# Performance work log

Measured on AMD Instinct MI355X. Metric: run time of the kernel, lower is better.

Reference implementation:

```python
import jax, jax.numpy as jnp
import numpy as np


def setup_inputs() -> dict:
    key = jax.random.key(0)
    k1, k2 = jax.random.split(key)
    num_tokens, top_k, num_experts = 1048576, 8, 64
    top_scores = jax.random.uniform(k1, (num_tokens, top_k), dtype=jnp.float32)
    selected_experts_indices = jax.random.randint(
        k2, (num_tokens, top_k), 0, num_experts, dtype=jnp.int64
    ) if jax.config.jax_enable_x64 else jax.random.randint(
        k2, (num_tokens, top_k), 0, num_experts, dtype=jnp.int32
    )
    return {
        "top_scores": top_scores,
        "selected_experts_indices": selected_experts_indices,
        "num_experts": num_experts,
    }


def reference(top_scores, selected_experts_indices, num_experts):
    flat_idx = selected_experts_indices.reshape(-1)  # [num_tokens*top_k]
    # histogram of tokens per expert (torch.histc returns float)
    num_tokens_per_expert = jnp.bincount(flat_idx, length=num_experts).astype(jnp.float32)
    # stable argsort by expert id -> permutation grouping tokens by expert
    token_indices_experts_sorted = jnp.argsort(flat_idx, stable=True)
    # gather routing scores into expert-sorted order
    top_scores_experts_sorted = top_scores.reshape(-1)[token_indices_experts_sorted]
    return (
        top_scores_experts_sorted,
        token_indices_experts_sorted,
        num_tokens_per_expert,
    )
```

## Files before the change

kernel.cpp:

```cpp
#include <hip/hip_runtime.h>


#define TILE 2048
#define WCH  512
#define RND  8

__device__ __forceinline__ unsigned long long match_mask(
    unsigned key,
    unsigned long long b0, unsigned long long b1, unsigned long long b2,
    unsigned long long b3, unsigned long long b4, unsigned long long b5,
    unsigned long long am) {
  unsigned long long m = am;
  m &= (key & 1u)  ? b0 : ~b0;
  m &= (key & 2u)  ? b1 : ~b1;
  m &= (key & 4u)  ? b2 : ~b2;
  m &= (key & 8u)  ? b3 : ~b3;
  m &= (key & 16u) ? b4 : ~b4;
  m &= (key & 32u) ? b5 : ~b5;
  return m;
}

__global__ __launch_bounds__(256) void hist_kernel(
    const int* __restrict__ idx, unsigned* __restrict__ countsT,
    int N, int nb) {
  __shared__ unsigned h[4][64];
  int wave = threadIdx.x >> 6;
  int lane = threadIdx.x & 63;
  h[wave][lane] = 0;
  __syncthreads();

  long long base = (long long)blockIdx.x * TILE;
  long long rem = (long long)N - base;
  if (rem >= TILE) {
    const int4* v = (const int4*)(idx + base);
    #pragma unroll
    for (int k = 0; k < TILE / 1024; ++k) {
      int4 x = v[threadIdx.x + k * 256];
      atomicAdd(&h[wave][((unsigned)x.x) & 63u], 1u);
      atomicAdd(&h[wave][((unsigned)x.y) & 63u], 1u);
      atomicAdd(&h[wave][((unsigned)x.z) & 63u], 1u);
      atomicAdd(&h[wave][((unsigned)x.w) & 63u], 1u);
    }
  } else if (rem > 0) {
    for (int j = threadIdx.x; j < (int)rem; j += 256)
      atomicAdd(&h[wave][((unsigned)idx[base + j]) & 63u], 1u);
  }
  __syncthreads();
  if (threadIdx.x < 64) {
    countsT[(size_t)threadIdx.x * nb + blockIdx.x] =
        h[0][threadIdx.x] + h[1][threadIdx.x] + h[2][threadIdx.x] + h[3][threadIdx.x];
  }
}

__global__ __launch_bounds__(256) void scan_kernel(
    unsigned* __restrict__ countsT, unsigned* __restrict__ totals,
    float* __restrict__ out_counts, int nb) {
  int e = blockIdx.x;
  int t = threadIdx.x;
  unsigned* row = countsT + (size_t)e * nb;
  int per = (nb + 255) >> 8;
  int base = t * per;

  unsigned s = 0;
  for (int j = 0; j < per; ++j) {
    int w = base + j;
    if (w < nb) s += row[w];
  }
  __shared__ unsigned sh[256];
  sh[t] = s;
  __syncthreads();
  for (int d = 1; d < 256; d <<= 1) {
    unsigned v = sh[t];
    unsigned a = (t >= d) ? sh[t - d] : 0u;
    __syncthreads();
    sh[t] = v + a;
    __syncthreads();
  }
  unsigned incl = sh[t];
  unsigned run = incl - s;
  for (int j = 0; j < per; ++j) {
    int w = base + j;
    if (w < nb) { unsigned v = row[w]; row[w] = run; run += v; }
  }
  if (t == 255) {
    totals[e] = incl;
    out_counts[e] = (float)incl;
  }
}

__global__ __launch_bounds__(256) void scatter_kernel(
    const int* __restrict__ idx, const float* __restrict__ scores,
    const unsigned* __restrict__ baseT, const unsigned* __restrict__ totals,
    float* __restrict__ out_scores, float* __restrict__ out_idx,
    int N, int nb) {
  __shared__ unsigned shc[4][64];
  __shared__ unsigned dbase[64];
  __shared__ float    ssc[TILE];
  __shared__ unsigned spk[TILE];

  const int wave = threadIdx.x >> 6;
  const int lane = threadIdx.x & 63;
  const unsigned long long lt = (1ull << lane) - 1ull;

  long long start = (long long)blockIdx.x * TILE + (long long)wave * WCH;
  long long remain = (long long)N - start;
  int full = 0;
  if (remain >= WCH) full = RND;
  else if (remain > 0) full = (int)(remain >> 6);
  bool hastail = (full < RND) && (remain > (long long)full * 64);

  unsigned rank_pk[2] = {0, 0};
  unsigned cnt_pk[2]  = {0, 0};
  unsigned e_pk[2]    = {0, 0};
  unsigned wtotal = 0;

  #pragma unroll
  for (int r = 0; r < RND; ++r) {
    if (r >= full) break;
    long long i = start + (long long)r * 64 + lane;
    unsigned e = ((unsigned)idx[i]) & 63u;
    unsigned long long b0 = __ballot(e & 1u);
    unsigned long long b1 = __ballot(e & 2u);
    unsigned long long b2 = __ballot(e & 4u);
    unsigned long long b3 = __ballot(e & 8u);
    unsigned long long b4 = __ballot(e & 16u);
    unsigned long long b5 = __ballot(e & 32u);
    unsigned long long ms = match_mask(e, b0, b1, b2, b3, b4, b5, ~0ull);
    unsigned long long ml = match_mask((unsigned)lane, b0, b1, b2, b3, b4, b5, ~0ull);
    unsigned rank = (unsigned)__popcll(ms & lt);
    unsigned cnt  = (unsigned)__popcll(ml);
    int q = r >> 2, sh = (r & 3) * 8;
    rank_pk[q] |= rank << sh;
    cnt_pk[q]  |= cnt << sh;
    e_pk[q]    |= e << sh;
    wtotal += cnt;
  }
  if (hastail) {
    int r = full;
    long long i = start + (long long)r * 64 + lane;
    bool valid = i < (long long)N;
    unsigned long long am = __ballot(valid ? 1 : 0);
    unsigned e = valid ? (((unsigned)idx[i]) & 63u) : 0u;
    unsigned long long b0 = __ballot(e & 1u);
    unsigned long long b1 = __ballot(e & 2u);
    unsigned long long b2 = __ballot(e & 4u);
    unsigned long long b3 = __ballot(e & 8u);
    unsigned long long b4 = __ballot(e & 16u);
    unsigned long long b5 = __ballot(e & 32u);
    unsigned long long ms = match_mask(e, b0, b1, b2, b3, b4, b5, am);
    unsigned long long ml = match_mask((unsigned)lane, b0, b1, b2, b3, b4, b5, am);
    unsigned rank = (unsigned)__popcll(ms & lt);
    unsigned cnt  = (unsigned)__popcll(ml);
    int q = r >> 2, sh = (r & 3) * 8;
    rank_pk[q] |= rank << sh;
    cnt_pk[q]  |= cnt << sh;
    e_pk[q]    |= e << sh;
    wtotal += cnt;
  }
  shc[wave][lane] = wtotal;
  __syncthreads();

  unsigned c0 = shc[0][lane], c1 = shc[1][lane], c2 = shc[2][lane], c3 = shc[3][lane];
  unsigned bc = c0 + c1 + c2 + c3;
  unsigned sum = bc;
  #pragma unroll
  for (int d = 1; d < 64; d <<= 1) {
    unsigned nv = __shfl_up(sum, d, 64);
    if (lane >= d) sum += nv;
  }
  unsigned local_start = sum - bc;
  unsigned running = local_start + (wave > 0 ? c0 : 0u) + (wave > 1 ? c1 : 0u) +
                     (wave > 2 ? c2 : 0u);

  if (threadIdx.x < 64) {
    unsigned tot = totals[lane];
    unsigned s2 = tot;
    #pragma unroll
    for (int d = 1; d < 64; d <<= 1) {
      unsigned nv = __shfl_up(s2, d, 64);
      if (lane >= d) s2 += nv;
    }
    unsigned estart = s2 - tot;
    unsigned gb0 = baseT[(size_t)lane * nb + blockIdx.x];
    dbase[lane] = estart + gb0 - local_start;
  }

  #pragma unroll
  for (int r = 0; r < RND; ++r) {
    if (r >= full) break;
    long long i = start + (long long)r * 64 + lane;
    float s = scores[i];
    int q = r >> 2, sh = (r & 3) * 8;
    unsigned e    = (e_pk[q] >> sh) & 0xffu;
    unsigned rank = (rank_pk[q] >> sh) & 0xffu;
    unsigned cnt  = (cnt_pk[q] >> sh) & 0xffu;
    unsigned old = (unsigned)__shfl((int)running, (int)e, 64);
    unsigned pos = old + rank;
    running += cnt;
    ssc[pos] = s;
    spk[pos] = (((unsigned)i) << 6) | e;
  }
  if (hastail) {
    int r = full;
    long long i = start + (long long)r * 64 + lane;
    bool valid = i < (long long)N;
    float s = valid ? scores[i] : 0.0f;
    int q = r >> 2, sh = (r & 3) * 8;
    unsigned e    = (e_pk[q] >> sh) & 0xffu;
    unsigned rank = (rank_pk[q] >> sh) & 0xffu;
    unsigned cnt  = (cnt_pk[q] >> sh) & 0xffu;
    unsigned old = (unsigned)__shfl((int)running, (int)e, 64);
    unsigned pos = old + rank;
    running += cnt;
    if (valid) {
      ssc[pos] = s;
      spk[pos] = (((unsigned)i) << 6) | e;
    }
  }
  __syncthreads();

  {
    long long bstart = (long long)blockIdx.x * TILE;
    long long rem = (long long)N - bstart;
    int bvalid = rem < TILE ? (int)rem : TILE;
    for (int j = threadIdx.x; j < bvalid; j += 256) {
      unsigned p = spk[j];
      unsigned e = p & 63u;
      unsigned d = dbase[e] + (unsigned)j;
      out_scores[d] = ssc[j];
      out_idx[d] = (float)(p >> 6);
    }
  }
}

extern "C" void kernel_launch(void* const* d_in, const int* in_sizes, int n_in,
                              void* d_out, int out_size, void* d_ws, size_t ws_size,
                              hipStream_t stream) {
  const float* scores = (const float*)d_in[0];
  const int* idx = (const int*)d_in[1];
  int N = in_sizes[0];

  float* out_scores = (float*)d_out;
  float* out_idx = out_scores + N;
  float* out_counts = out_idx + N;

  int nb = (N + TILE - 1) / TILE;
  unsigned* countsT = (unsigned*)d_ws;
  unsigned* totals = countsT + (size_t)64 * nb;

  hist_kernel<<<nb, 256, 0, stream>>>(idx, countsT, N, nb);
  scan_kernel<<<64, 256, 0, stream>>>(countsT, totals, out_counts, nb);
  scatter_kernel<<<nb, 256, 0, stream>>>(idx, scores, countsT, totals,
                                         out_scores, out_idx, N, nb);
}
```

Before: 158.7 us.

## Scatter into per-wave local segments to drop mid-kernel block barrier

The scatter kernel now has each wave lay out its own 512-element segment of shared memory sorted by expert, using only an intra-wave prefix scan. The block-wide histogram combine moves after the local scatter, and the per-wave/per-expert destination offsets go into a 4x64 table. This removes one __syncthreads between the ranking and local-scatter phases and lets waves proceed independently. It also adds launch_bounds occupancy 8 and a fast path for full tiles. The cost is an extra wave scan and table lookup, and the global writes become less contiguous because runs are split per wave.

```diff
diff --git a/kernel.cpp b/kernel.cpp
--- a/kernel.cpp
+++ b/kernel.cpp
@@ -88,91 +88,125 @@
   }
 }
 
-__global__ __launch_bounds__(256) void scatter_kernel(
+__global__ __launch_bounds__(256, 8) void scatter_kernel(
     const int* __restrict__ idx, const float* __restrict__ scores,
     const unsigned* __restrict__ baseT, const unsigned* __restrict__ totals,
     float* __restrict__ out_scores, float* __restrict__ out_idx,
     int N, int nb) {
-  __shared__ unsigned shc[4][64];
-  __shared__ unsigned dbase[64];
   __shared__ float    ssc[TILE];
   __shared__ unsigned spk[TILE];
+  __shared__ unsigned shc[4][64];
+  __shared__ unsigned table[4][64];
 
   const int wave = threadIdx.x >> 6;
   const int lane = threadIdx.x & 63;
   const unsigned long long lt = (1ull << lane) - 1ull;
 
-  long long start = (long long)blockIdx.x * TILE + (long long)wave * WCH;
-  long long remain = (long long)N - start;
-  int full = 0;
-  if (remain >= WCH) full = RND;
-  else if (remain > 0) full = (int)(remain >> 6);
-  bool hastail = (full < RND) && (remain > (long long)full * 64);
+  const long long start = (long long)blockIdx.x * TILE + (long long)wave * WCH;
+  const bool fullt = ((long long)(blockIdx.x + 1) * TILE) <= (long long)N;
 
   unsigned rank_pk[2] = {0, 0};
   unsigned cnt_pk[2]  = {0, 0};
   unsigned e_pk[2]    = {0, 0};
   unsigned wtotal = 0;
 
-  #pragma unroll
-  for (int r = 0; r < RND; ++r) {
-    if (r >= full) break;
-    long long i = start + (long long)r * 64 + lane;
-    unsigned e = ((unsigned)idx[i]) & 63u;
-    unsigned long long b0 = __ballot(e & 1u);
-    unsigned long long b1 = __ballot(e & 2u);
-    unsigned long long b2 = __ballot(e & 4u);
-    unsigned long long b3 = __ballot(e & 8u);
-    unsigned long long b4 = __ballot(e & 16u);
-    unsigned long long b5 = __ballot(e & 32u);
-    unsigned long long ms = match_mask(e, b0, b1, b2, b3, b4, b5, ~0ull);
-    unsigned long long ml = match_mask((unsigned)lane, b0, b1, b2, b3, b4, b5, ~0ull);
-    unsigned rank = (unsigned)__popcll(ms & lt);
-    unsigned cnt  = (unsigned)__popcll(ml);
-    int q = r >> 2, sh = (r & 3) * 8;
-    rank_pk[q] |= rank << sh;
-    cnt_pk[q]  |= cnt << sh;
-    e_pk[q]    |= e << sh;
-    wtotal += cnt;
-  }
-  if (hastail) {
-    int r = full;
-    long long i = start + (long long)r * 64 + lane;
-    bool valid = i < (long long)N;
-    unsigned long long am = __ballot(valid ? 1 : 0);
-    unsigned e = valid ? (((unsigned)idx[i]) & 63u) : 0u;
-    unsigned long long b0 = __ballot(e & 1u);
-    unsigned long long b1 = __ballot(e & 2u);
-    unsigned long long b2 = __ballot(e & 4u);
-    unsigned long long b3 = __ballot(e & 8u);
-    unsigned long long b4 = __ballot(e & 16u);
-    unsigned long long b5 = __ballot(e & 32u);
-    unsigned long long ms = match_mask(e, b0, b1, b2, b3, b4, b5, am);
-    unsigned long long ml = match_mask((unsigned)lane, b0, b1, b2, b3, b4, b5, am);
-    unsigned rank = (unsigned)__popcll(ms & lt);
-    unsigned cnt  = (unsigned)__popcll(ml);
-    int q = r >> 2, sh = (r & 3) * 8;
-    rank_pk[q] |= rank << sh;
-    cnt_pk[q]  |= cnt << sh;
-    e_pk[q]    |= e << sh;
-    wtotal += cnt;
-  }
-  shc[wave][lane] = wtotal;
-  __syncthreads();
-
-  unsigned c0 = shc[0][lane], c1 = shc[1][lane], c2 = shc[2][lane], c3 = shc[3][lane];
-  unsigned bc = c0 + c1 + c2 + c3;
-  unsigned sum = bc;
+  if (fullt) {
+    #pragma unroll
+    for (int r = 0; r < RND; ++r) {
+      long long i = start + r * 64 + lane;
+      unsigned e = ((unsigned)idx[i]) & 63u;
+      unsigned long long b0 = __ballot(e & 1u);
+      unsigned long long b1 = __ballot(e & 2u);
+      unsigned long long b2 = __ballot(e & 4u);
+      unsigned long long b3 = __ballot(e & 8u);
+      unsigned long long b4 = __ballot(e & 16u);
+      unsigned long long b5 = __ballot(e & 32u);
+      unsigned long long ms = match_mask(e, b0, b1, b2, b3, b4, b5, ~0ull);
+      unsigned long long ml = match_mask((unsigned)lane, b0, b1, b2, b3, b4, b5, ~0ull);
+      unsigned rank = (unsigned)__popcll(ms & lt);
+      unsigned cnt  = (unsigned)__popcll(ml);
+      const int q = r >> 2, sh = (r & 3) * 8;
+      rank_pk[q] |= rank << sh;
+      cnt_pk[q]  |= cnt << sh;
+      e_pk[q]    |= e << sh;
+      wtotal += cnt;
+    }
+  } else {
+    for (int j = threadIdx.x; j < TILE; j += 256) spk[j] = 0xFFFFFFFFu;
+    __syncthreads();
+    for (int r = 0; r < RND; ++r) {
+      long long i = start + (long long)r * 64 + lane;
+      bool valid = i < (long long)N;
+      unsigned long long am = __ballot(valid ? 1 : 0);
+      unsigned e = valid ? (((unsigned)idx[i]) & 63u) : 0u;
+      unsigned long long b0 = __ballot(e & 1u);
+      unsigned long long b1 = __ballot(e & 2u);
+      unsigned long long b2 = __ballot(e & 4u);
+      unsigned long long b3 = __ballot(e & 8u);
+      unsigned long long b4 = __ballot(e & 16u);
+      unsigned long long b5 = __ballot(e & 32u);
+      unsigned long long ms = match_mask(e, b0, b1, b2, b3, b4, b5, am);
+      unsigned long long ml = match_mask((unsigned)lane, b0, b1, b2, b3, b4, b5, am);
+      unsigned rank = (unsigned)__popcll(ms & lt);
+      unsigned cnt  = (unsigned)__popcll(ml);
+      const int q = r >> 2, sh = (r & 3) * 8;
+      rank_pk[q] |= rank << sh;
+      cnt_pk[q]  |= cnt << sh;
+      e_pk[q]    |= (valid ? e : 0u) << sh;
+      wtotal += cnt;
+    }
+  }
+
+  unsigned sum = wtotal;
   #pragma unroll
   for (int d = 1; d < 64; d <<= 1) {
     unsigned nv = __shfl_up(sum, d, 64);
     if (lane >= d) sum += nv;
   }
-  unsigned local_start = sum - bc;
-  unsigned running = local_start + (wave > 0 ? c0 : 0u) + (wave > 1 ? c1 : 0u) +
-                     (wave > 2 ? c2 : 0u);
-
-  if (threadIdx.x < 64) {
+  unsigned ws_l = (unsigned)(wave * WCH) + (sum - wtotal);
+
+  unsigned cur[RND];
+  {
+    unsigned acc = ws_l;
+    #pragma unroll
+    for (int r = 0; r < RND; ++r) {
+      cur[r] = acc;
+      acc += (cnt_pk[r >> 2] >> ((r & 3) * 8)) & 0xffu;
+    }
+  }
+
+  if (fullt) {
+    #pragma unroll
+    for (int r = 0; r < RND; ++r) {
+      long long i = start + r * 64 + lane;
+      float s = scores[i];
+      const int q = r >> 2, sh = (r & 3) * 8;
+      unsigned e    = (e_pk[q] >> sh) & 0xffu;
+      unsigned rank = (rank_pk[q] >> sh) & 0xffu;
+      unsigned pos = (unsigned)__shfl((int)cur[r], (int)e, 64) + rank;
+      ssc[pos] = s;
+      spk[pos] = (((unsigned)i) << 6) | e;
+    }
+  } else {
+    for (int r = 0; r < RND; ++r) {
+      long long i = start + (long long)r * 64 + lane;
+      bool valid = i < (long long)N;
+      float s = valid ? scores[i] : 0.0f;
+      const int q = r >> 2, sh = (r & 3) * 8;
+      unsigned e    = (e_pk[q] >> sh) & 0xffu;
+      unsigned rank = (rank_pk[q] >> sh) & 0xffu;
+      unsigned pos = (unsigned)__shfl((int)cur[r], (int)e, 64) + rank;
+      if (valid) {
+        ssc[pos] = s;
+        spk[pos] = (((unsigned)i) << 6) | e;
+      }
+    }
+  }
+
+  shc[wave][lane] = wtotal;
+  __syncthreads();
+
+  {
     unsigned tot = totals[lane];
     unsigned s2 = tot;
     #pragma unroll
@@ -182,51 +216,39 @@
     }
     unsigned estart = s2 - tot;
     unsigned gb0 = baseT[(size_t)lane * nb + blockIdx.x];
-    dbase[lane] = estart + gb0 - local_start;
-  }
-
-  #pragma unroll
-  for (int r = 0; r < RND; ++r) {
-    if (r >= full) break;
-    long long i = start + (long long)r * 64 + lane;
-    float s = scores[i];
-    int q = r >> 2, sh = (r & 3) * 8;
-    unsigned e    = (e_pk[q] >> sh) & 0xffu;
-    unsigned rank = (rank_pk[q] >> sh) & 0xffu;
-    unsigned cnt  = (cnt_pk[q] >> sh) & 0xffu;
-    unsigned old = (unsigned)__shfl((int)running, (int)e, 64);
-    unsigned pos = old + rank;
-    running += cnt;
-    ssc[pos] = s;
-    spk[pos] = (((unsigned)i) << 6) | e;
-  }
-  if (hastail) {
-    int r = full;
-    long long i = start + (long long)r * 64 + lane;
-    bool valid = i < (long long)N;
-    float s = valid ? scores[i] : 0.0f;
-    int q = r >> 2, sh = (r & 3) * 8;
-    unsigned e    = (e_pk[q] >> sh) & 0xffu;
-    unsigned rank = (rank_pk[q] >> sh) & 0xffu;
-    unsigned cnt  = (cnt_pk[q] >> sh) & 0xffu;
-    unsigned old = (unsigned)__shfl((int)running, (int)e, 64);
-    unsigned pos = old + rank;
-    running += cnt;
-    if (valid) {
-      ssc[pos] = s;
-      spk[pos] = (((unsigned)i) << 6) | e;
-    }
-  }
-  __syncthreads();
-
-  {
-    long long bstart = (long long)blockIdx.x * TILE;
-    long long rem = (long long)N - bstart;
-    int bvalid = rem < TILE ? (int)rem : TILE;
-    for (int j = threadIdx.x; j < bvalid; j += 256) {
+
+    unsigned c = shc[wave][lane];
+    unsigned s3 = c;
+    #pragma unroll
+    for (int d = 1; d < 64; d <<= 1) {
+      unsigned nv = __shfl_up(s3, d, 64);
+      if (lane >= d) s3 += nv;
+    }
+    unsigned wse = (unsigned)(wave * WCH) + (s3 - c);
+
+    unsigned wpre = 0;
+    for (int w2 = 0; w2 < wave; ++w2) wpre += shc[w2][lane];
+
+    table[wave][lane] = estart + gb0 + wpre - wse;
+  }
+  __syncthreads();
+
+  if (fullt) {
+    for (int j = threadIdx.x; j < TILE; j += 256) {
       unsigned p = spk[j];
       unsigned e = p & 63u;
-      unsigned d = dbase[e] + (unsigned)j;
+      int w = j >> 9;
+      unsigned d = table[w][e] + (unsigned)j;
+      out_scores[d] = ssc[j];
+      out_idx[d] = (float)(p >> 6);
+    }
+  } else {
+    for (int j = threadIdx.x; j < TILE; j += 256) {
+      unsigned p = spk[j];
+      if (p == 0xFFFFFFFFu) continue;
+      unsigned e = p & 63u;
+      int w = j >> 9;
+      unsigned d = table[w][e] + (unsigned)j;
       out_scores[d] = ssc[j];
       out_idx[d] = (float)(p >> 6);
     }
```

New measurement: 158.5 us. Within noise of the previous version (-0.1%).
